# Performance work log

Measured on AMD Instinct MI355X. Metric: run time of the kernel, lower is better.

The kernel has to match this reference:

```python
import jax, jax.numpy as jnp
import numpy as np

NB_SAMPLES = 16
GAMMA = 0.04       # also the noise_intensity passed to randomArgmax
ALPHA = 1.0
EPS = 1e-10


def setup_inputs() -> dict:
    key = jax.random.key(0)
    k1, k2, k3 = jax.random.split(key, 3)
    B, H, W, K = 8, 128, 128, 32
    zbuf = jax.random.normal(k1, (B, H, W, K), dtype=jnp.float32)
    prob_map = jax.random.uniform(k2, (B, H, W, K), dtype=jnp.float32)
    mask = jnp.ones((B, H, W, K), dtype=jnp.float32)
    zfar = jnp.ones((1,), dtype=jnp.float32)
    znear = jnp.zeros((1,), dtype=jnp.float32)
    # gaussian noise normally drawn inside randomArgmax.forward; made explicit for determinism
    noise = jax.random.normal(k3, (NB_SAMPLES, B, H, W, K + 1), dtype=jnp.float32)
    return {"zbuf": zbuf, "zfar": zfar, "znear": znear,
            "prob_map": prob_map, "mask": mask, "noise": noise}


def _random_argmax(z, noise, sigma):
    # z: [B,H,W,C]; noise: [S,B,H,W,C]
    C = z.shape[-1]
    z_pert = z[None] + sigma * noise                       # [S,B,H,W,C]
    idx = jnp.argmax(z_pert, axis=-1)                      # first-max, matches torch.max
    weights = jax.nn.one_hot(idx, C, dtype=z.dtype)        # [S,B,H,W,C]
    return weights.mean(axis=0)                            # [B,H,W,C]


def reference(zbuf, zfar, znear, prob_map, mask, noise):
    # inverse depth, masked
    z_inv = (zfar - zbuf) / (zfar - znear) * mask          # [B,H,W,K]
    z_inv_max = jnp.maximum(jnp.max(z_inv, axis=-1, keepdims=True), EPS)
    z_map = GAMMA / ALPHA * jnp.log(1e-12 + prob_map) + z_inv - z_inv_max
    bg = EPS - z_inv_max                                   # background channel [B,H,W,1]
    z_map = jnp.concatenate([z_map, bg], axis=-1)          # [B,H,W,K+1]
    return _random_argmax(z_map, noise, GAMMA)
```

## Files before the change

kernel.cpp:

```cpp
#include <hip/hip_runtime.h>


#define NPIX   (8 * 128 * 128)
#define KCH    32
#define CCH    33
#define SAMP   16
#define TPB    256
#define TILE   (TPB * CCH)

__global__ __launch_bounds__(TPB)
void gauss_agg_kernel(const float* __restrict__ zbuf,
                      const float* __restrict__ zfar_p,
                      const float* __restrict__ znear_p,
                      const float* __restrict__ prob,
                      const float* __restrict__ mask,
                      const float* __restrict__ noise,
                      float* __restrict__ out)
{
#pragma clang fp contract(off)
    __shared__ float lds[TILE];
    const int tid = threadIdx.x;
    const int p0  = blockIdx.x * TPB;
    const size_t p = (size_t)p0 + tid;

    const float zfar  = zfar_p[0];
    const float znear = znear_p[0];
    const float denom = zfar - znear;

    float zb[KCH], pm[KCH], mk[KCH];
    {
        const float4* zb4 = reinterpret_cast<const float4*>(zbuf + p * KCH);
        const float4* pm4 = reinterpret_cast<const float4*>(prob + p * KCH);
        const float4* mk4 = reinterpret_cast<const float4*>(mask + p * KCH);
        #pragma unroll
        for (int i = 0; i < KCH / 4; ++i) {
            float4 a = zb4[i], b = pm4[i], c = mk4[i];
            zb[4*i+0] = a.x; zb[4*i+1] = a.y; zb[4*i+2] = a.z; zb[4*i+3] = a.w;
            pm[4*i+0] = b.x; pm[4*i+1] = b.y; pm[4*i+2] = b.z; pm[4*i+3] = b.w;
            mk[4*i+0] = c.x; mk[4*i+1] = c.y; mk[4*i+2] = c.z; mk[4*i+3] = c.w;
        }
    }

    float z_inv[KCH];
    float zmax = 1e-10f;
    #pragma unroll
    for (int k = 0; k < KCH; ++k) {
        float zi = ((zfar - zb[k]) / denom) * mk[k];
        z_inv[k] = zi;
        zmax = fmaxf(zmax, zi);
    }

    float z_map[CCH];
    #pragma unroll
    for (int k = 0; k < KCH; ++k) {
        float lg = logf(1e-12f + pm[k]);
        z_map[k] = ((0.04f * lg) + z_inv[k]) - zmax;
    }
    z_map[KCH] = 1e-10f - zmax;

    int acc[CCH];
    #pragma unroll
    for (int c = 0; c < CCH; ++c) acc[c] = 0;

    for (int s = 0; s < SAMP; ++s) {
        __syncthreads();
        {
            const float4* g4 = reinterpret_cast<const float4*>(
                noise + ((size_t)s * NPIX + p0) * CCH);
            float4* l4 = reinterpret_cast<float4*>(lds);
            for (int i = tid; i < TILE / 4; i += TPB) l4[i] = g4[i];
        }
        __syncthreads();

        const int base = tid * CCH;
        float best = z_map[0] + (0.04f * lds[base + 0]);
        int bi = 0;
        #pragma unroll
        for (int c = 1; c < CCH; ++c) {
            float v = z_map[c] + (0.04f * lds[base + c]);
            if (v > best) { best = v; bi = c; }
        }
        #pragma unroll
        for (int c = 0; c < CCH; ++c) acc[c] += (bi == c) ? 1 : 0;
    }

    __syncthreads();
    {
        const int base = tid * CCH;
        #pragma unroll
        for (int c = 0; c < CCH; ++c)
            lds[base + c] = (float)acc[c] * 0.0625f;
    }
    __syncthreads();
    {
        const float4* l4 = reinterpret_cast<const float4*>(lds);
        float4* o4 = reinterpret_cast<float4*>(out + (size_t)p0 * CCH);
        for (int i = tid; i < TILE / 4; i += TPB) o4[i] = l4[i];
    }
}

extern "C" void kernel_launch(void* const* d_in, const int* in_sizes, int n_in,
                              void* d_out, int out_size, void* d_ws, size_t ws_size,
                              hipStream_t stream)
{
    const float* zbuf  = (const float*)d_in[0];
    const float* zfar  = (const float*)d_in[1];
    const float* znear = (const float*)d_in[2];
    const float* prob  = (const float*)d_in[3];
    const float* mask  = (const float*)d_in[4];
    const float* noise = (const float*)d_in[5];
    float* out = (float*)d_out;

    dim3 grid(NPIX / TPB), block(TPB);
    gauss_agg_kernel<<<grid, block, 0, stream>>>(zbuf, zfar, znear, prob, mask,
                                                 noise, out);
}
```

Baseline: 428.5 us.

## Prefetch next sample's noise tile into registers while computing current argmax

```diff
diff --git a/kernel.cpp b/kernel.cpp
--- a/kernel.cpp
+++ b/kernel.cpp
@@ -1,12 +1,16 @@
 #include <hip/hip_runtime.h>
+#include <cstdint>
 
 
-#define NPIX   (8 * 128 * 128)
-#define KCH    32
-#define CCH    33
-#define SAMP   16
-#define TPB    256
-#define TILE   (TPB * CCH)
+#define NPIX    131072
+#define KCH     32
+#define CCH     33
+#define SAMP    16
+#define TPB     128
+#define TILE_F  (TPB * CCH)
+#define TILE_V4 (TILE_F / 4)
+#define FULL_J  (TILE_V4 / TPB)
+#define REM     (TILE_V4 % TPB)
 
 __global__ __launch_bounds__(TPB)
 void gauss_agg_kernel(const float* __restrict__ zbuf,
@@ -18,7 +22,7 @@
                       float* __restrict__ out)
 {
 #pragma clang fp contract(off)
-    __shared__ float lds[TILE];
+    __shared__ float buf[TILE_F];
     const int tid = threadIdx.x;
     const int p0  = blockIdx.x * TPB;
     const size_t p = (size_t)p0 + tid;
@@ -39,6 +43,15 @@
             pm[4*i+0] = b.x; pm[4*i+1] = b.y; pm[4*i+2] = b.z; pm[4*i+3] = b.w;
             mk[4*i+0] = c.x; mk[4*i+1] = c.y; mk[4*i+2] = c.z; mk[4*i+3] = c.w;
         }
+    }
+
+    float4 r[FULL_J + 1];
+    {
+        const float4* g4 = reinterpret_cast<const float4*>(
+            noise + (size_t)p0 * CCH);
+        #pragma unroll
+        for (int j = 0; j < FULL_J; ++j) r[j] = g4[tid + j * TPB];
+        if (tid < REM) r[FULL_J] = g4[tid + FULL_J * TPB];
     }
 
     float z_inv[KCH];
@@ -63,39 +76,45 @@
     for (int c = 0; c < CCH; ++c) acc[c] = 0;
 
     for (int s = 0; s < SAMP; ++s) {
-        __syncthreads();
+        if (s) __syncthreads();
         {
-            const float4* g4 = reinterpret_cast<const float4*>(
-                noise + ((size_t)s * NPIX + p0) * CCH);
-            float4* l4 = reinterpret_cast<float4*>(lds);
-            for (int i = tid; i < TILE / 4; i += TPB) l4[i] = g4[i];
+            float4* l4 = reinterpret_cast<float4*>(buf);
+            #pragma unroll
+            for (int j = 0; j < FULL_J; ++j) l4[tid + j * TPB] = r[j];
+            if (tid < REM) l4[tid + FULL_J * TPB] = r[FULL_J];
         }
         __syncthreads();
-
-        const int base = tid * CCH;
-        float best = z_map[0] + (0.04f * lds[base + 0]);
+        if (s + 1 < SAMP) {
+            const float4* g4 = reinterpret_cast<const float4*>(
+                noise + ((size_t)(s + 1) * NPIX + p0) * CCH);
+            #pragma unroll
+            for (int j = 0; j < FULL_J; ++j) r[j] = g4[tid + j * TPB];
+            if (tid < REM) r[FULL_J] = g4[tid + FULL_J * TPB];
+        }
+        const float* nb = buf + tid * CCH;
+        float best = z_map[0] + (0.04f * nb[0]);
         int bi = 0;
         #pragma unroll
         for (int c = 1; c < CCH; ++c) {
-            float v = z_map[c] + (0.04f * lds[base + c]);
+            float v = z_map[c] + (0.04f * nb[c]);
             if (v > best) { best = v; bi = c; }
         }
         #pragma unroll
-        for (int c = 0; c < CCH; ++c) acc[c] += (bi == c) ? 1 : 0;
+        for (int c = 0; c < CCH; ++c) acc[c] += (bi == c);
     }
 
-    __syncthreads();
     {
-        const int base = tid * CCH;
+        const int rb = tid * CCH;
         #pragma unroll
-        for (int c = 0; c < CCH; ++c)
-            lds[base + c] = (float)acc[c] * 0.0625f;
+        for (int c = 0; c < CCH; ++c) buf[rb + c] = (float)acc[c] * 0.0625f;
     }
     __syncthreads();
     {
-        const float4* l4 = reinterpret_cast<const float4*>(lds);
+        const float4* l4 = reinterpret_cast<const float4*>(buf);
         float4* o4 = reinterpret_cast<float4*>(out + (size_t)p0 * CCH);
-        for (int i = tid; i < TILE / 4; i += TPB) o4[i] = l4[i];
+        #pragma unroll
+        for (int j = 0; j < FULL_J; ++j) o4[tid + j * TPB] = l4[tid + j * TPB];
+        if (tid < REM) o4[tid + FULL_J * TPB] = l4[tid + FULL_J * TPB];
     }
 }
 
```

After: 442.6 us. +3.3%, slower.
